# Kernel optimization log

Hardware: AMD Instinct MI355X
Metric: run time of the kernel (lower is better)

Reference implementation:

```python
import jax, jax.numpy as jnp
import numpy as np

B, HIDDEN, NH, MAX_S = 8, 4096, 32, 4096
HD = HIDDEN // NH  # 128
POS = 2047  # current cache write position (tokens 0..POS-1 already cached)


def setup_inputs() -> dict:
    key = jax.random.key(0)
    ks = jax.random.split(key, 7)
    x = jax.random.normal(ks[0], (B, 1, HIDDEN), dtype=jnp.float32)
    cached_k = jax.random.normal(ks[1], (B, NH, MAX_S, HD), dtype=jnp.float32)
    cached_v = jax.random.normal(ks[2], (B, NH, MAX_S, HD), dtype=jnp.float32)
    scale = 0.02
    wq = jax.random.normal(ks[3], (HIDDEN, HIDDEN), dtype=jnp.float32) * scale
    wk = jax.random.normal(ks[4], (HIDDEN, HIDDEN), dtype=jnp.float32) * scale
    wv = jax.random.normal(ks[5], (HIDDEN, HIDDEN), dtype=jnp.float32) * scale
    wo = jax.random.normal(ks[6], (HIDDEN, HIDDEN), dtype=jnp.float32) * scale
    return {"x": x, "cached_k": cached_k, "cached_v": cached_v,
            "wq": wq, "wk": wk, "wv": wv, "wo": wo, "cached_pos": POS}


def reference(x, cached_k, cached_v, wq, wk, wv, wo, cached_pos):
    # Decode step: seq_len == 1 (is_training=False path of the torch module).
    b, s, hidden = x.shape  # s == 1
    # Projections (torch Linear: y = x @ W.T), reshape to [B, H, 1, D]
    q = (x @ wq.T).reshape(b, s, NH, HD).transpose(0, 2, 1, 3)
    k = (x @ wk.T).reshape(b, s, NH, HD).transpose(0, 2, 1, 3)
    v = (x @ wv.T).reshape(b, s, NH, HD).transpose(0, 2, 1, 3)
    # Append new token's K/V into the cache at cached_pos (static python int)
    ck = cached_k.at[:, :, cached_pos, :].set(k[:, :, 0, :])
    cv = cached_v.at[:, :, cached_pos, :].set(v[:, :, 0, :])
    # Attend over the valid prefix [0, cached_pos]
    kk = ck[:, :, :cached_pos + 1, :]  # [B, H, T, D]
    vv = cv[:, :, :cached_pos + 1, :]
    scores = jnp.einsum('bhqd,bhkd->bhqk', q, kk) / jnp.sqrt(jnp.float32(HD))
    att = jax.nn.softmax(scores, axis=-1)  # stable softmax == module's _softmax
    out = jnp.einsum('bhqk,bhkd->bhqd', att, vv)  # [B, H, 1, D]
    out = out.transpose(0, 2, 1, 3).reshape(b, s, hidden)
    return out @ wo.T
```

## Files before the change

kernel.cpp:

```cpp
#include <hip/hip_runtime.h>
#include <cmath>

#define B_     8
#define NH_    32
#define HD_    128
#define HID_   4096
#define MAXS_  4096
#define NPAIR_ (B_ * NH_)
#define NSPLIT_ 4
#define PSTR_  132
#define NEG_BIG_ (-1e30f)

typedef float f4_ __attribute__((ext_vector_type(4)));

__device__ __forceinline__ f4_ ntload4(const float* p) {
  return __builtin_nontemporal_load((const f4_*)p);
}
__device__ __forceinline__ f4_ ld4(const float* p) {
  return *(const f4_*)p;
}
__device__ __forceinline__ float dot4(f4_ a, f4_ b) {
  f4_ m = a * b;
  return m.x + m.y + m.z + m.w;
}

template<int NSL>
__global__ __launch_bounds__(64) void gemv8p(
    const float* __restrict__ W0, const float* __restrict__ W1,
    const float* __restrict__ W2, const float* __restrict__ x,
    float* __restrict__ out, int nb_per_mat, int n_inner, int part_stride)
{
  const int bid   = blockIdx.x;
  const int ks    = bid / n_inner;
  const int inner = bid % n_inner;
  const int m     = inner / nb_per_mat;
  const int r0    = (inner % nb_per_mat) * 8;
  const float* __restrict__ W = (m == 0) ? W0 : ((m == 1) ? W1 : W2);
  float* o = out + (size_t)ks * part_stride + m * (B_ * HID_);

  const int lane = threadIdx.x;
  const int kofs = ks * NSL * 256;

  float acc[8][8];
#pragma unroll
  for (int r = 0; r < 8; ++r)
#pragma unroll
    for (int b = 0; b < 8; ++b) acc[r][b] = 0.f;

  const float* Wp = W + (size_t)r0 * HID_ + kofs + lane * 4;
  const float* xp = x + kofs + lane * 4;

  f4_ wa[8], wb[8], xa[8], xb[8];
#pragma unroll
  for (int r = 0; r < 8; ++r) wa[r] = ld4(Wp + (size_t)r * HID_);
#pragma unroll
  for (int b = 0; b < 8; ++b) xa[b] = ld4(xp + b * HID_);

#pragma unroll 1
  for (int u = 0; u < NSL; u += 2) {
    {
      const int j1 = (u + 1) * 256;
#pragma unroll
      for (int r = 0; r < 8; ++r) wb[r] = ld4(Wp + (size_t)r * HID_ + j1);
#pragma unroll
      for (int b = 0; b < 8; ++b) xb[b] = ld4(xp + b * HID_ + j1);
#pragma unroll
      for (int r = 0; r < 8; ++r)
#pragma unroll
        for (int b = 0; b < 8; ++b) acc[r][b] += dot4(wa[r], xa[b]);
    }
    {
      if (u + 2 < NSL) {
        const int j2 = (u + 2) * 256;
#pragma unroll
        for (int r = 0; r < 8; ++r) wa[r] = ld4(Wp + (size_t)r * HID_ + j2);
#pragma unroll
        for (int b = 0; b < 8; ++b) xa[b] = ld4(xp + b * HID_ + j2);
      }
#pragma unroll
      for (int r = 0; r < 8; ++r)
#pragma unroll
        for (int b = 0; b < 8; ++b) acc[r][b] += dot4(wb[r], xb[b]);
    }
  }

#pragma unroll
  for (int r = 0; r < 8; ++r)
#pragma unroll
    for (int b = 0; b < 8; ++b) {
      float v = acc[r][b];
#pragma unroll
      for (int off = 32; off; off >>= 1) v += __shfl_xor(v, off);
      acc[r][b] = v;
    }

  if (lane == 0) {
#pragma unroll
    for (int r = 0; r < 8; ++r)
#pragma unroll
      for (int b = 0; b < 8; ++b)
        o[(size_t)b * HID_ + r0 + r] = acc[r][b];
  }
}

__global__ __launch_bounds__(256) void sum4(
    const float* __restrict__ part, float* __restrict__ out)
{
  const int gid = blockIdx.x * 256 + threadIdx.x;
  const int i = gid * 4;
  f4_ v = ld4(part + i) + ld4(part + (B_ * HID_) + i)
        + ld4(part + 2 * (B_ * HID_) + i) + ld4(part + 3 * (B_ * HID_) + i);
  *(f4_*)(out + i) = v;
}

__global__ __launch_bounds__(256, 4) void attn_partial(
    const float* __restrict__ qkv, const float* __restrict__ ck,
    const float* __restrict__ cv, const int* __restrict__ ppos,
    float* __restrict__ part)
{
  __shared__ float sm[4], sl[4];
  __shared__ float sacc[4][HD_];

  const int pos  = *ppos;
  const int bid  = blockIdx.x;
  const int pair = bid >> 2;
  const int s    = bid & (NSPLIT_ - 1);
  const int b    = pair >> 5;
  const int h    = pair & (NH_ - 1);
  const int w    = threadIdx.x >> 6;
  const int lane = threadIdx.x & 63;
  const int half = lane >> 5, l32 = lane & 31;
  const int k0   = s * 512 + w * 128;

  float m = NEG_BIG_, l = 0.f;
  f4_ acc = (f4_)0.f;

  if (k0 <= pos) {
    const float scale = 0.08838834764831845f;
    const int hoff = b * HID_ + h * HD_ + l32 * 4;
    f4_ q4  = ld4(qkv + hoff) * scale;
    f4_ kf4 = ld4(qkv + B_ * HID_ + hoff);
    f4_ vf4 = ld4(qkv + 2 * B_ * HID_ + hoff);
    const float* ckh = ck + ((size_t)(b * NH_ + h)) * MAXS_ * HD_;
    const float* cvh = cv + ((size_t)(b * NH_ + h)) * MAXS_ * HD_;

    for (int c = 0; c < 8; ++c) {
      const int kbase = k0 + c * 16;
      f4_ k4[8], v4[8];
#pragma unroll
      for (int j = 0; j < 8; ++j) {
        const int ki = kbase + 2 * j + half;
        k4[j] = ntload4(ckh + (size_t)ki * HD_ + l32 * 4);
        v4[j] = ntload4(cvh + (size_t)ki * HD_ + l32 * 4);
      }
#pragma unroll
      for (int j = 0; j < 8; ++j) {
        const int ki = kbase + 2 * j + half;
        if (ki == pos) { k4[j] = kf4; v4[j] = vf4; }
      }

      float sc[8];
#pragma unroll
      for (int j = 0; j < 8; ++j) sc[j] = dot4(q4, k4[j]);

#pragma unroll
      for (int off = 16; off >= 1; off >>= 1)
#pragma unroll
        for (int j = 0; j < 8; ++j) sc[j] += __shfl_xor(sc[j], off);

#pragma unroll
      for (int j = 0; j < 8; ++j) {
        const int ki = kbase + 2 * j + half;
        if (ki > pos) sc[j] = -INFINITY;
      }

      const float cm = fmaxf(fmaxf(fmaxf(sc[0], sc[1]), fmaxf(sc[2], sc[3])),
                             fmaxf(fmaxf(sc[4], sc[5]), fmaxf(sc[6], sc[7])));
      const float mn   = fmaxf(m, cm);
      const float corr = __expf(m - mn);
      float p[8], ps = 0.f;
#pragma unroll
      for (int j = 0; j < 8; ++j) { p[j] = __expf(sc[j] - mn); ps += p[j]; }
      l = l * corr + ps;
      acc *= corr;
#pragma unroll
      for (int j = 0; j < 8; ++j) acc += p[j] * v4[j];
      m = mn;
    }
  }

  const float mo = __shfl_xor(m, 32);
  const float lo = __shfl_xor(l, 32);
  f4_ ao;
  ao.x = __shfl_xor(acc.x, 32); ao.y = __shfl_xor(acc.y, 32);
  ao.z = __shfl_xor(acc.z, 32); ao.w = __shfl_xor(acc.w, 32);
  const float mm = fmaxf(m, mo);
  const float w0 = __expf(m - mm), w1 = __expf(mo - mm);
  const float lm = l * w0 + lo * w1;
  f4_ am = acc * w0 + ao * w1;

  if (half == 0) {
    *(f4_*)&sacc[w][l32 * 4] = am;
    if (l32 == 0) { sm[w] = mm; sl[w] = lm; }
  }
  __syncthreads();

  if (threadIdx.x < 32) {
    const int t = threadIdx.x;
    float mg = NEG_BIG_;
#pragma unroll
    for (int u = 0; u < 4; ++u)
      if (sl[u] > 0.f) mg = fmaxf(mg, sm[u]);
    float ls = 0.f;
    f4_ o = (f4_)0.f;
#pragma unroll
    for (int u = 0; u < 4; ++u)
      if (sl[u] > 0.f) {
        const float wu = __expf(sm[u] - mg);
        ls += sl[u] * wu;
        o  += wu * ld4(&sacc[u][t * 4]);
      }
    float* pb = part + (size_t)bid * PSTR_;
    *(f4_*)(pb + 4 + t * 4) = o;
    if (t == 0) { pb[0] = (ls > 0.f) ? mg : NEG_BIG_; pb[1] = ls; }
  }
}

__global__ __launch_bounds__(128) void attn_combine(
    const float* __restrict__ part, float* __restrict__ attnout)
{
  const int pair = blockIdx.x;
  const int d    = threadIdx.x;
  const float* pb = part + (size_t)pair * NSPLIT_ * PSTR_;

  float mg = NEG_BIG_;
#pragma unroll
  for (int u = 0; u < NSPLIT_; ++u) {
    const float lu = pb[u * PSTR_ + 1];
    if (lu > 0.f) mg = fmaxf(mg, pb[u * PSTR_]);
  }
  float ls = 0.f, o = 0.f;
#pragma unroll
  for (int u = 0; u < NSPLIT_; ++u) {
    const float lu = pb[u * PSTR_ + 1];
    if (lu > 0.f) {
      const float wu = __expf(pb[u * PSTR_] - mg);
      ls += lu * wu;
      o  += wu * pb[u * PSTR_ + 4 + d];
    }
  }
  attnout[pair * HD_ + d] = o / ls;
}

extern "C" void kernel_launch(void* const* d_in, const int* in_sizes, int n_in,
                              void* d_out, int out_size, void* d_ws, size_t ws_size,
                              hipStream_t stream) {
  const float* x  = (const float*)d_in[0];
  const float* ck = (const float*)d_in[1];
  const float* cv = (const float*)d_in[2];
  const float* wq = (const float*)d_in[3];
  const float* wk = (const float*)d_in[4];
  const float* wv = (const float*)d_in[5];
  const float* wo = (const float*)d_in[6];
  const int* pos  = (const int*)d_in[7];
  float* out = (float*)d_out;
  float* ws  = (float*)d_ws;

  float* qkv     = ws;
  float* part    = qkv + 3 * B_ * HID_;
  float* attnout = part + NPAIR_ * NSPLIT_ * PSTR_;
  float* wopart  = attnout + B_ * HID_;

  gemv8p<16><<<3 * 512, 64, 0, stream>>>(wq, wk, wv, x, qkv,
                                         512, 3 * 512, 0);
  attn_partial<<<NPAIR_ * NSPLIT_, 256, 0, stream>>>(qkv, ck, cv, pos, part);
  attn_combine<<<NPAIR_, 128, 0, stream>>>(part, attnout);
  gemv8p<4><<<4 * 512, 64, 0, stream>>>(wo, wo, wo, attnout, wopart,
                                        512, 512, B_ * HID_);
  sum4<<<(B_ * HID_) / (256 * 4), 256, 0, stream>>>(wopart, out);
}
```

Baseline: 176.5 us.

## Fuse split-K attention and combine into one 512-thread block per head pair

Drops the 4-way key split across blocks plus the separate combine kernel. Each (batch, head) pair now gets a single 512-thread block whose 8 waves each cover 256 keys, merged in shared memory, with the normalized output written directly. This removes one kernel launch and the global round trip of partial results. In exchange the attention grid shrinks from 1024 blocks to 256, which lowers parallelism and may reduce how well the KV-cache stream saturates memory bandwidth across the CUs.

```diff
diff --git a/kernel.cpp b/kernel.cpp
--- a/kernel.cpp
+++ b/kernel.cpp
@@ -7,8 +7,6 @@
 #define HID_   4096
 #define MAXS_  4096
 #define NPAIR_ (B_ * NH_)
-#define NSPLIT_ 4
-#define PSTR_  132
 #define NEG_BIG_ (-1e30f)
 
 typedef float f4_ __attribute__((ext_vector_type(4)));
@@ -113,24 +111,22 @@
   *(f4_*)(out + i) = v;
 }
 
-__global__ __launch_bounds__(256, 4) void attn_partial(
+__global__ __launch_bounds__(512) void attn_pair(
     const float* __restrict__ qkv, const float* __restrict__ ck,
     const float* __restrict__ cv, const int* __restrict__ ppos,
-    float* __restrict__ part)
+    float* __restrict__ attnout)
 {
-  __shared__ float sm[4], sl[4];
-  __shared__ float sacc[4][HD_];
+  __shared__ float sm[8], sl[8];
+  __shared__ float sacc[8][HD_];
 
   const int pos  = *ppos;
-  const int bid  = blockIdx.x;
-  const int pair = bid >> 2;
-  const int s    = bid & (NSPLIT_ - 1);
+  const int pair = blockIdx.x;
   const int b    = pair >> 5;
   const int h    = pair & (NH_ - 1);
   const int w    = threadIdx.x >> 6;
   const int lane = threadIdx.x & 63;
   const int half = lane >> 5, l32 = lane & 31;
-  const int k0   = s * 512 + w * 128;
+  const int k0   = w * 256;
 
   float m = NEG_BIG_, l = 0.f;
   f4_ acc = (f4_)0.f;
@@ -144,7 +140,7 @@
     const float* ckh = ck + ((size_t)(b * NH_ + h)) * MAXS_ * HD_;
     const float* cvh = cv + ((size_t)(b * NH_ + h)) * MAXS_ * HD_;
 
-    for (int c = 0; c < 8; ++c) {
+    for (int c = 0; c < 16; ++c) {
       const int kbase = k0 + c * 16;
       f4_ k4[8], v4[8];
 #pragma unroll
@@ -209,47 +205,19 @@
     const int t = threadIdx.x;
     float mg = NEG_BIG_;
 #pragma unroll
-    for (int u = 0; u < 4; ++u)
+    for (int u = 0; u < 8; ++u)
       if (sl[u] > 0.f) mg = fmaxf(mg, sm[u]);
     float ls = 0.f;
     f4_ o = (f4_)0.f;
 #pragma unroll
-    for (int u = 0; u < 4; ++u)
+    for (int u = 0; u < 8; ++u)
       if (sl[u] > 0.f) {
         const float wu = __expf(sm[u] - mg);
         ls += sl[u] * wu;
         o  += wu * ld4(&sacc[u][t * 4]);
       }
-    float* pb = part + (size_t)bid * PSTR_;
-    *(f4_*)(pb + 4 + t * 4) = o;
-    if (t == 0) { pb[0] = (ls > 0.f) ? mg : NEG_BIG_; pb[1] = ls; }
-  }
-}
-
-__global__ __launch_bounds__(128) void attn_combine(
-    const float* __restrict__ part, float* __restrict__ attnout)
-{
-  const int pair = blockIdx.x;
-  const int d    = threadIdx.x;
-  const float* pb = part + (size_t)pair * NSPLIT_ * PSTR_;
-
-  float mg = NEG_BIG_;
-#pragma unroll
-  for (int u = 0; u < NSPLIT_; ++u) {
-    const float lu = pb[u * PSTR_ + 1];
-    if (lu > 0.f) mg = fmaxf(mg, pb[u * PSTR_]);
-  }
-  float ls = 0.f, o = 0.f;
-#pragma unroll
-  for (int u = 0; u < NSPLIT_; ++u) {
-    const float lu = pb[u * PSTR_ + 1];
-    if (lu > 0.f) {
-      const float wu = __expf(pb[u * PSTR_] - mg);
-      ls += lu * wu;
-      o  += wu * pb[u * PSTR_ + 4 + d];
-    }
-  }
-  attnout[pair * HD_ + d] = o / ls;
+    *(f4_*)(attnout + pair * HD_ + t * 4) = o / ls;
+  }
 }
 
 extern "C" void kernel_launch(void* const* d_in, const int* in_sizes, int n_in,
@@ -267,14 +235,12 @@
   float* ws  = (float*)d_ws;
 
   float* qkv     = ws;
-  float* part    = qkv + 3 * B_ * HID_;
-  float* attnout = part + NPAIR_ * NSPLIT_ * PSTR_;
+  float* attnout = qkv + 3 * B_ * HID_;
   float* wopart  = attnout + B_ * HID_;
 
   gemv8p<16><<<3 * 512, 64, 0, stream>>>(wq, wk, wv, x, qkv,
                                          512, 3 * 512, 0);
-  attn_partial<<<NPAIR_ * NSPLIT_, 256, 0, stream>>>(qkv, ck, cv, pos, part);
-  attn_combine<<<NPAIR_, 128, 0, stream>>>(part, attnout);
+  attn_pair<<<NPAIR_, 512, 0, stream>>>(qkv, ck, cv, pos, attnout);
   gemv8p<4><<<4 * 512, 64, 0, stream>>>(wo, wo, wo, attnout, wopart,
                                         512, 512, B_ * HID_);
   sum4<<<(B_ * HID_) / (256 * 4), 256, 0, stream>>>(wopart, out);
```

Measured after the change: 176.4 us. About the same (-0.1%).
